# Optimization experiments

Hardware: AMD Instinct MI355X
Metric: run time of the kernel (lower is better)

The kernel has to match this reference:

```python
import jax, jax.numpy as jnp
import numpy as np

N_NODES = 100000
K_NEIGH = 32
N_IN = 64
N_OUT = 64


def setup_inputs() -> dict:
    key = jax.random.key(0)
    k1, k2, k3 = jax.random.split(key, 3)
    x = jax.random.normal(k1, (N_NODES, K_NEIGH, N_IN), dtype=jnp.float32)
    # Linear params (torch Linear: y = x @ W.T + b; we store W as [n_in, n_out])
    W = jax.random.normal(k2, (N_IN, N_OUT), dtype=jnp.float32) * (1.0 / np.sqrt(N_IN))
    b = jax.random.normal(k3, (N_OUT,), dtype=jnp.float32) * 0.01
    return {"x": x, "W": W, "b": b}


def reference(x, W, b):
    # x: [N, K, n_in] per-edge features grouped by node
    h = jax.nn.relu(jnp.einsum("nki,io->nko", x, W) + b)  # Linear + ReLU per edge
    return jnp.max(h, axis=1)  # max-pool over neighbors -> [N, n_out]
```

## Files before the change

kernel.cpp:

```cpp
#include <hip/hip_runtime.h>
#include <hip/hip_bf16.h>


typedef __attribute__((ext_vector_type(8))) short bf16x8;
typedef __attribute__((ext_vector_type(4))) float f32x4;

#define KNEIGH 32
#define NIN 64
#define NOUT 64

__device__ __forceinline__ short f2bf(float f) {
    __hip_bfloat16 h = __float2bfloat16(f);
    return __builtin_bit_cast(short, h);
}

__global__ __launch_bounds__(256) void edge_mfma_kernel(
    const float* __restrict__ x, const float* __restrict__ W,
    const float* __restrict__ b, float* __restrict__ out,
    int n_nodes, int wave_stride)
{
    const int lane = threadIdx.x & 63;
    const int l16  = lane & 15;
    const int lg   = lane >> 4;

    bf16x8 Wf[4][2];
#pragma unroll
    for (int t = 0; t < 4; ++t) {
#pragma unroll
        for (int s = 0; s < 2; ++s) {
#pragma unroll
            for (int j = 0; j < 8; ++j) {
                int k = s * 32 + lg * 8 + j;
                int o = t * 16 + l16;
                Wf[t][s][j] = f2bf(W[k * NOUT + o]);
            }
        }
    }
    float bias[4];
#pragma unroll
    for (int t = 0; t < 4; ++t) bias[t] = b[t * 16 + l16];

    const int wave = blockIdx.x * (blockDim.x >> 6) + (threadIdx.x >> 6);

    for (int n = wave; n < n_nodes; n += wave_stride) {
        const float* xb = x + (size_t)n * (KNEIGH * NIN);

        f32x4 xr[2][2][2];
#pragma unroll
        for (int m = 0; m < 2; ++m) {
#pragma unroll
            for (int s = 0; s < 2; ++s) {
                const f32x4* p = reinterpret_cast<const f32x4*>(
                    xb + (m * 16 + l16) * NIN + s * 32 + lg * 8);
                xr[m][s][0] = __builtin_nontemporal_load(p);
                xr[m][s][1] = __builtin_nontemporal_load(p + 1);
            }
        }

        bf16x8 Af[2][2];
#pragma unroll
        for (int m = 0; m < 2; ++m) {
#pragma unroll
            for (int s = 0; s < 2; ++s) {
#pragma unroll
                for (int j = 0; j < 4; ++j) {
                    Af[m][s][j]     = f2bf(xr[m][s][0][j]);
                    Af[m][s][4 + j] = f2bf(xr[m][s][1][j]);
                }
            }
        }

        f32x4 acc[2][4];
#pragma unroll
        for (int m = 0; m < 2; ++m)
#pragma unroll
            for (int t = 0; t < 4; ++t)
                acc[m][t] = (f32x4){0.f, 0.f, 0.f, 0.f};

#pragma unroll
        for (int m = 0; m < 2; ++m) {
#pragma unroll
            for (int t = 0; t < 4; ++t) {
                acc[m][t] = __builtin_amdgcn_mfma_f32_16x16x32_bf16(
                    Af[m][0], Wf[t][0], acc[m][t], 0, 0, 0);
                acc[m][t] = __builtin_amdgcn_mfma_f32_16x16x32_bf16(
                    Af[m][1], Wf[t][1], acc[m][t], 0, 0, 0);
            }
        }

        float res[4];
#pragma unroll
        for (int t = 0; t < 4; ++t) {
            float v0 = fmaxf(acc[0][t][0], acc[1][t][0]);
            float v1 = fmaxf(acc[0][t][1], acc[1][t][1]);
            float v2 = fmaxf(acc[0][t][2], acc[1][t][2]);
            float v3 = fmaxf(acc[0][t][3], acc[1][t][3]);
            float r = fmaxf(fmaxf(v0, v1), fmaxf(v2, v3));
            r = fmaxf(r, __shfl_xor(r, 16));
            r = fmaxf(r, __shfl_xor(r, 32));
            res[t] = fmaxf(r + bias[t], 0.0f);
        }

        float val = (lg == 0) ? res[0] : (lg == 1) ? res[1] : (lg == 2) ? res[2] : res[3];
        __builtin_nontemporal_store(val, &out[(size_t)n * NOUT + lane]);
    }
}

extern "C" void kernel_launch(void* const* d_in, const int* in_sizes, int n_in,
                              void* d_out, int out_size, void* d_ws, size_t ws_size,
                              hipStream_t stream) {
    const float* x = (const float*)d_in[0];
    const float* W = (const float*)d_in[1];
    const float* b = (const float*)d_in[2];
    float* out = (float*)d_out;

    const int n_nodes = in_sizes[0] / (KNEIGH * NIN);
    const int blocks = 2048;
    const int wave_stride = blocks * 4;

    hipLaunchKernelGGL(edge_mfma_kernel, dim3(blocks), dim3(256), 0, stream,
                       x, W, b, out, n_nodes, wave_stride);
}
```

Baseline: 194.2 us.

## Prefetch next node's features into LDS via async global_load_lds

Result: faster. 165.7 us (-14.7%).

```diff
diff --git a/kernel.cpp b/kernel.cpp
--- a/kernel.cpp
+++ b/kernel.cpp
@@ -8,20 +8,31 @@
 #define KNEIGH 32
 #define NIN 64
 #define NOUT 64
+#define NODE_ELTS (KNEIGH * NIN)
 
 __device__ __forceinline__ short f2bf(float f) {
     __hip_bfloat16 h = __float2bfloat16(f);
     return __builtin_bit_cast(short, h);
 }
 
-__global__ __launch_bounds__(256) void edge_mfma_kernel(
+__device__ __forceinline__ void gload16(const float* gsrc, float* lds_base) {
+    __builtin_amdgcn_global_load_lds(
+        (const __attribute__((address_space(1))) unsigned int*)gsrc,
+        (__attribute__((address_space(3))) unsigned int*)lds_base, 16, 0, 0);
+}
+
+__global__ __launch_bounds__(256, 4) void edge_mfma_kernel(
     const float* __restrict__ x, const float* __restrict__ W,
     const float* __restrict__ b, float* __restrict__ out,
     int n_nodes, int wave_stride)
 {
+    __shared__ float lds[4][NODE_ELTS];
+
     const int lane = threadIdx.x & 63;
     const int l16  = lane & 15;
     const int lg   = lane >> 4;
+    const int wid  = threadIdx.x >> 6;
+    float* my = lds[wid];
 
     bf16x8 Wf[4][2];
 #pragma unroll
@@ -40,22 +51,52 @@
 #pragma unroll
     for (int t = 0; t < 4; ++t) bias[t] = b[t * 16 + l16];
 
-    const int wave = blockIdx.x * (blockDim.x >> 6) + (threadIdx.x >> 6);
+    int goff[8];
+#pragma unroll
+    for (int i = 0; i < 8; ++i) {
+        int r = i * 4 + lg;
+        int cu = l16 ^ (r & 15);
+        goff[i] = r * 64 + cu * 4;
+    }
 
-    for (int n = wave; n < n_nodes; n += wave_stride) {
-        const float* xb = x + (size_t)n * (KNEIGH * NIN);
+    const int S = wave_stride;
+    int n = blockIdx.x * 4 + wid;
+    if (n >= n_nodes) return;
 
-        f32x4 xr[2][2][2];
+    {
+        const float* xb = x + (size_t)n * NODE_ELTS;
+#pragma unroll
+        for (int i = 0; i < 8; ++i) gload16(xb + goff[i], my + i * 256);
+    }
+
+    for (; n < n_nodes; n += S) {
+        const int nn = n + S;
+
+        asm volatile("s_waitcnt vmcnt(0)" ::: "memory");
+        __builtin_amdgcn_sched_barrier(0);
+
+        f32x4 q[2][2][2];
 #pragma unroll
         for (int m = 0; m < 2; ++m) {
 #pragma unroll
             for (int s = 0; s < 2; ++s) {
-                const f32x4* p = reinterpret_cast<const f32x4*>(
-                    xb + (m * 16 + l16) * NIN + s * 32 + lg * 8);
-                xr[m][s][0] = __builtin_nontemporal_load(p);
-                xr[m][s][1] = __builtin_nontemporal_load(p + 1);
+#pragma unroll
+                for (int w = 0; w < 2; ++w) {
+                    int r = m * 16 + l16;
+                    int u = (s * 8 + lg * 2 + w) ^ l16;
+                    q[m][s][w] = *reinterpret_cast<const f32x4*>(my + r * 64 + u * 4);
+                }
             }
         }
+        asm volatile("s_waitcnt lgkmcnt(0)" ::: "memory");
+        __builtin_amdgcn_sched_barrier(0);
+
+        if (nn < n_nodes) {
+            const float* xb = x + (size_t)nn * NODE_ELTS;
+#pragma unroll
+            for (int i = 0; i < 8; ++i) gload16(xb + goff[i], my + i * 256);
+        }
+        __builtin_amdgcn_sched_barrier(0);
 
         bf16x8 Af[2][2];
 #pragma unroll
@@ -63,9 +104,9 @@
 #pragma unroll
             for (int s = 0; s < 2; ++s) {
 #pragma unroll
-                for (int j = 0; j < 4; ++j) {
-                    Af[m][s][j]     = f2bf(xr[m][s][0][j]);
-                    Af[m][s][4 + j] = f2bf(xr[m][s][1][j]);
+                for (int jj = 0; jj < 4; ++jj) {
+                    Af[m][s][jj]     = f2bf(q[m][s][0][jj]);
+                    Af[m][s][4 + jj] = f2bf(q[m][s][1][jj]);
                 }
             }
         }
@@ -102,7 +143,7 @@
         }
 
         float val = (lg == 0) ? res[0] : (lg == 1) ? res[1] : (lg == 2) ? res[2] : res[3];
-        __builtin_nontemporal_store(val, &out[(size_t)n * NOUT + lane]);
+        out[(size_t)n * NOUT + lane] = val;
     }
 }
 
@@ -115,7 +156,7 @@
     float* out = (float*)d_out;
 
     const int n_nodes = in_sizes[0] / (KNEIGH * NIN);
-    const int blocks = 2048;
+    const int blocks = 1000;
     const int wave_stride = blocks * 4;
 
     hipLaunchKernelGGL(edge_mfma_kernel, dim3(blocks), dim3(256), 0, stream,
```
